# Performance work log

Measured on AMD Instinct MI355X. Metric: run time of the kernel, lower is better.

The kernel has to match this reference:

```python
import math
import jax, jax.numpy as jnp
import numpy as np

B, T, C, H = 1, 2048, 1024, 16
D = C // H
ROPE_THETA = 10000.0


def rope_sin_cos(t, d, theta, dtype=jnp.float32):
    # (T, D/2) sin/cos tables, standard RoPE frequencies
    inv_freq = 1.0 / (theta ** (jnp.arange(0, d, 2, dtype=jnp.float32) / d))
    ang = jnp.arange(t, dtype=jnp.float32)[:, None] * inv_freq[None, :]  # (T, D/2)
    return jnp.sin(ang).astype(dtype), jnp.cos(ang).astype(dtype)


def apply_rope(x, sin, cos):
    # x: (B, H, T, D); rotate interleaved even/odd pairs
    x1 = x[..., 0::2]
    x2 = x[..., 1::2]
    s = sin[None, None, :, :]
    c = cos[None, None, :, :]
    r1 = x1 * c - x2 * s
    r2 = x1 * s + x2 * c
    # interleave back to (..., D)
    return jnp.stack([r1, r2], axis=-1).reshape(x.shape)


def setup_inputs() -> dict:
    key = jax.random.key(0)
    k1, k2, k3 = jax.random.split(key, 3)
    x = jax.random.normal(k1, (B, T, C), dtype=jnp.float32)
    w_qkv = jax.random.normal(k2, (C, 3 * C), dtype=jnp.float32) * (1.0 / math.sqrt(C))
    w_proj = jax.random.normal(k3, (C, C), dtype=jnp.float32) * (1.0 / math.sqrt(C))
    return {"x": x, "w_qkv": w_qkv, "w_proj": w_proj}


def reference(x, w_qkv, w_proj):
    b, t, c = x.shape
    qkv = x @ w_qkv                               # (B, T, 3C)
    qkv = qkv.reshape(b, t, 3, H, D)
    q = qkv[:, :, 0].transpose(0, 2, 1, 3)        # (B, H, T, D)
    k = qkv[:, :, 1].transpose(0, 2, 1, 3)
    v = qkv[:, :, 2].transpose(0, 2, 1, 3)

    sin, cos = rope_sin_cos(t, D, ROPE_THETA, dtype=x.dtype)
    q = apply_rope(q, sin, cos)
    k = apply_rope(k, sin, cos)

    scores = jnp.einsum('bhqd,bhkd->bhqk', q, k) * (1.0 / math.sqrt(D))
    causal = jnp.tril(jnp.ones((t, t), dtype=bool))
    scores = jnp.where(causal[None, None, :, :], scores, jnp.finfo(scores.dtype).min)
    probs = jax.nn.softmax(scores, axis=-1)       # (B, H, T, T)
    out = jnp.einsum('bhqk,bhkd->bhqd', probs, v)
    out = out.transpose(0, 2, 1, 3).reshape(b, t, c)
    return out @ w_proj
```

## Files before the change

kernel.cpp:

```cpp
#include <hip/hip_runtime.h>
#include <math.h>

#define TT 2048
#define CC 1024
#define HH 16
#define DD 64
#define N3 3072

typedef unsigned short u16;
typedef __bf16 bf16x8 __attribute__((ext_vector_type(8)));
typedef float f32x4 __attribute__((ext_vector_type(4)));
typedef unsigned short u16x8 __attribute__((ext_vector_type(8)));
typedef const __attribute__((address_space(1))) void gv_t;
typedef __attribute__((address_space(3))) void lv_t;

__device__ __forceinline__ u16 bf16_rne(float f) {
  unsigned u = __float_as_uint(f);
  u += 0x7FFFu + ((u >> 16) & 1u);
  return (u16)(u >> 16);
}
__device__ __forceinline__ float bf16f(u16 h) {
  return __uint_as_float(((unsigned)h) << 16);
}
__device__ __forceinline__ bf16x8 ldfrag(const u16* p) {
  return __builtin_bit_cast(bf16x8, *(const u16x8*)p);
}
#if __has_builtin(__builtin_amdgcn_cvt_pk_bf16_f32)
__device__ __forceinline__ unsigned pk_bf16(float a, float b) {
  return __builtin_bit_cast(unsigned, __builtin_amdgcn_cvt_pk_bf16_f32(a, b));
}
#else
__device__ __forceinline__ unsigned pk_bf16(float a, float b) {
  return (unsigned)bf16_rne(a) | ((unsigned)bf16_rne(b) << 16);
}
#endif

__global__ __launch_bounds__(256) void k_prep(
    const float* __restrict__ x, const float* __restrict__ w_qkv,
    const float* __restrict__ w_proj, u16* __restrict__ xb,
    u16* __restrict__ wqkvT, u16* __restrict__ wprojT,
    float2* __restrict__ scos ) {
  __shared__ u16 tile[64][34];
  const int bi = blockIdx.x, tid = threadIdx.x;
  if (bi < 2048) {
    int i = bi * 256 + tid;
    float4 v = ((const float4*)x)[i];
    ushort4 r;
    r.x = bf16_rne(v.x); r.y = bf16_rne(v.y); r.z = bf16_rne(v.z); r.w = bf16_rne(v.w);
    ((ushort4*)xb)[i] = r;
    return;
  }
  if (bi >= 2048 + 1536 + 512) {
    int idx = (bi - 4096) * 256 + tid;
    int t = idx >> 5, i = idx & 31;
    float inv_freq = exp2f(-(float)(2 * i) * (1.0f / 64.0f) * 13.2877123795494f);
    float ang = (float)t * inv_freq;
    scos[idx] = make_float2(sinf(ang), cosf(ang));
    return;
  }
  const float* w; u16* wt; int K, N, n0, k0;
  if (bi < 2048 + 1536) {
    int b = bi - 2048; w = w_qkv; wt = wqkvT; K = CC; N = N3;
    k0 = (b / 96) * 64; n0 = (b % 96) * 32;
  } else {
    int b = bi - 3584; w = w_proj; wt = wprojT; K = CC; N = CC;
    k0 = (b >> 5) * 64; n0 = (b & 31) * 32;
  }
  const int tx = tid & 31, r0 = tid >> 5;
#pragma unroll
  for (int j = 0; j < 8; j++) {
    int k = r0 + j * 8;
    tile[k][tx] = bf16_rne(w[(size_t)(k0 + k) * N + n0 + tx]);
  }
  __syncthreads();
  const int kc = tid & 15, nr = tid >> 4;
#pragma unroll
  for (int jn = 0; jn < 2; jn++) {
    int n = nr + (jn << 4);
    ushort4 o;
    o.x = tile[kc * 4 + 0][n];
    o.y = tile[kc * 4 + 1][n];
    o.z = tile[kc * 4 + 2][n];
    o.w = tile[kc * 4 + 3][n];
    *(ushort4*)&wt[(size_t)(n0 + n) * K + k0 + kc * 4] = o;
  }
}

__device__ __forceinline__ bf16x8 rdsw(const u16* base, int rr, int c8) {
  return ldfrag(&base[rr * 64 + ((c8 ^ (rr & 7)) << 3)]);
}

__global__ __launch_bounds__(256) void k_gemm_qkv(
    const u16* __restrict__ A, const u16* __restrict__ Bt,
    const float2* __restrict__ scos , u16* __restrict__ qr,
    u16* __restrict__ kr, u16* __restrict__ vt, int M, int N, int K) {
  __shared__ u16 As[2][128 * 64];
  __shared__ u16 Bs[2][96 * 64];
  const int tid = threadIdx.x;
  const int lane = tid & 63, w = tid >> 6;
  const int col = lane & 15, quad = lane >> 4;
  const int wm = w >> 1, wn = w & 1;
  const int tm = blockIdx.y * 128, tn = blockIdx.x * 96;

  const int lr = lane >> 3;
  const int soff = ((lane & 7) ^ lr) << 3;

  f32x4 acc[12];
#pragma unroll
  for (int i = 0; i < 12; i++) acc[i] = (f32x4){0.f, 0.f, 0.f, 0.f};

  auto stage = [&](int k0, int buf) {
#pragma unroll
    for (int i = 0; i < 4; i++) {
      const int rbase = w * 32 + i * 8;
      __builtin_amdgcn_global_load_lds(
          (gv_t*)(A + (size_t)(tm + rbase + lr) * K + k0 + soff),
          (lv_t*)(&As[buf][rbase * 64]), 16, 0, 0);
    }
#pragma unroll
    for (int i = 0; i < 3; i++) {
      const int rbase = w * 24 + i * 8;
      __builtin_amdgcn_global_load_lds(
          (gv_t*)(Bt + (size_t)(tn + rbase + lr) * K + k0 + soff),
          (lv_t*)(&Bs[buf][rbase * 64]), 16, 0, 0);
    }
  };

  stage(0, 0);
  __syncthreads();
  const int NT = K / 64;
  for (int t = 0; t < NT; t++) {
    const int cur = t & 1;
    if (t + 1 < NT) stage((t + 1) * 64, cur ^ 1);
#pragma unroll
    for (int kk = 0; kk < 2; kk++) {
      bf16x8 af[4], bf[3];
#pragma unroll
      for (int mt = 0; mt < 4; mt++)
        af[mt] = rdsw(&As[cur][0], wm * 64 + mt * 16 + col, kk * 4 + quad);
#pragma unroll
      for (int nt = 0; nt < 3; nt++)
        bf[nt] = rdsw(&Bs[cur][0], wn * 48 + nt * 16 + col, kk * 4 + quad);
#pragma unroll
      for (int mt = 0; mt < 4; mt++)
#pragma unroll
        for (int nt = 0; nt < 3; nt++)
          acc[mt * 3 + nt] = __builtin_amdgcn_mfma_f32_16x16x32_bf16(af[mt], bf[nt], acc[mt * 3 + nt], 0, 0, 0);
    }
    __syncthreads();
  }
  u16* scr = ((u16*)As) + w * 1088;

  const int tb = tm + wm * 64;
#pragma unroll
  for (int nt = 0; nt < 3; nt++) {
    const int nn = tn + wn * 48 + nt * 16;
    const int slice = nn >> 10;
    const int hh = (nn >> 6) & 15;
    const int db = nn & 63;
    const int d = db + col;
    if (slice < 2) {
      u16* dst = (slice == 0) ? qr : kr;
      const bool ev = (col & 1) == 0;
      const int i = (db >> 1) + (col >> 1);
#pragma unroll
      for (int mt = 0; mt < 4; mt++)
#pragma unroll
        for (int r = 0; r < 4; r++) {
          int t = tb + mt * 16 + quad * 4 + r;
          float2 sc2 = scos[t * 32 + i];
          float e = acc[mt * 3 + nt][r];
          float pp = __shfl_xor(e, 1);
          float v = ev ? (e * sc2.y - pp * sc2.x) : (pp * sc2.x + e * sc2.y);
          dst[((size_t)(hh * TT + t) << 6) + d] = bf16_rne(v);
        }
    } else {
#pragma unroll
      for (int mt = 0; mt < 4; mt++)
#pragma unroll
        for (int r = 0; r < 4; r++)
          scr[col * 68 + mt * 16 + quad * 4 + r] = bf16_rne(acc[mt * 3 + nt][r]);
#pragma unroll
      for (int i = 0; i < 4; i++) {
        const int dl = quad + i * 4;
        const int tl = col * 4;
        ushort4 vv = *(const ushort4*)&scr[dl * 68 + tl];
        *(ushort4*)&vt[((size_t)(hh * DD + db + dl)) * TT + tb + tl] = vv;
      }
    }
  }
}

__global__ __launch_bounds__(256) void k_gemm_pj(
    const u16* __restrict__ A, const u16* __restrict__ Bt,
    float* __restrict__ C, int M, int N, int K) {
  __shared__ u16 As[2][64 * 64];
  __shared__ u16 Bs[2][64 * 64];
  const int tid = threadIdx.x;
  const int lane = tid & 63, w = tid >> 6;
  const int col = lane & 15, quad = lane >> 4;
  const int wm = w >> 1, wn = w & 1;
  const int tm = blockIdx.y * 64, tn = blockIdx.x * 64;

  const int lr = lane >> 3;
  const int soff = ((lane & 7) ^ lr) << 3;

  f32x4 acc[4];
#pragma unroll
  for (int i = 0; i < 4; i++) acc[i] = (f32x4){0.f, 0.f, 0.f, 0.f};

  auto stage = [&](int k0, int buf) {
#pragma unroll
    for (int i = 0; i < 2; i++) {
      const int rbase = w * 16 + i * 8;
      __builtin_amdgcn_global_load_lds(
          (gv_t*)(A + (size_t)(tm + rbase + lr) * K + k0 + soff),
          (lv_t*)(&As[buf][rbase * 64]), 16, 0, 0);
      __builtin_amdgcn_global_load_lds(
          (gv_t*)(Bt + (size_t)(tn + rbase + lr) * K + k0 + soff),
          (lv_t*)(&Bs[buf][rbase * 64]), 16, 0, 0);
    }
  };

  stage(0, 0);
  __syncthreads();
  const int NT = K / 64;
  for (int t = 0; t < NT; t++) {
    const int cur = t & 1;
    if (t + 1 < NT) stage((t + 1) * 64, cur ^ 1);
#pragma unroll
    for (int kk = 0; kk < 2; kk++) {
      bf16x8 af[2], bf[2];
#pragma unroll
      for (int mt = 0; mt < 2; mt++)
        af[mt] = rdsw(&As[cur][0], wm * 32 + mt * 16 + col, kk * 4 + quad);
#pragma unroll
      for (int nt = 0; nt < 2; nt++)
        bf[nt] = rdsw(&Bs[cur][0], wn * 32 + nt * 16 + col, kk * 4 + quad);
#pragma unroll
      for (int mt = 0; mt < 2; mt++)
#pragma unroll
        for (int nt = 0; nt < 2; nt++)
          acc[mt * 2 + nt] = __builtin_amdgcn_mfma_f32_16x16x32_bf16(af[mt], bf[nt], acc[mt * 2 + nt], 0, 0, 0);
    }
    __syncthreads();
  }
#pragma unroll
  for (int mt = 0; mt < 2; mt++)
#pragma unroll
    for (int nt = 0; nt < 2; nt++)
#pragma unroll
      for (int r = 0; r < 4; r++)
        C[(size_t)(tm + wm * 32 + mt * 16 + quad * 4 + r) * N + tn + wn * 32 + nt * 16 + col] =
            acc[mt * 2 + nt][r];
}

__global__ __launch_bounds__(256) void k_flash(
    const u16* __restrict__ qr, const u16* __restrict__ kr,
    const u16* __restrict__ vt, u16* __restrict__ attnb ) {
  __shared__ u16 Ks[2][64 * 64];
  __shared__ u16 Vs[2][64 * 64];
  __shared__ u16 Ps[4][16 * 64];

  const int tid = threadIdx.x;
  const int lane = tid & 63, wv = tid >> 6;
  const int col = lane & 15, quad = lane >> 4;

  const int bid = blockIdx.x;
  const int xcd = bid & 7, slot = bid >> 3;
  const int cu = slot & 31, half = slot >> 5;
  const int rank = half ? (63 - cu) : cu;
  const int sp = 31 - (rank >> 1);
  const int h = xcd * 2 + (rank & 1);
  const int q0 = sp * 64;
  const int nkt = sp + 1;

  const u16* Qh = qr + (size_t)h * TT * DD;
  const u16* Kh = kr + (size_t)h * TT * DD;
  const u16* Vh = vt + (size_t)h * DD * TT;

  const bf16x8 aq0 = ldfrag(&Qh[(size_t)(q0 + wv * 16 + col) * DD + quad * 8]);
  const bf16x8 aq1 = ldfrag(&Qh[(size_t)(q0 + wv * 16 + col) * DD + 32 + quad * 8]);

  const int lr = lane >> 3;
  const int srcoff = ((lane & 7) ^ lr) << 3;

  auto stage = [&](int j, int buf) {
    const int k0 = j * 64;
#pragma unroll
    for (int i = 0; i < 2; i++) {
      const int rbase = wv * 16 + i * 8;
      __builtin_amdgcn_global_load_lds(
          (gv_t*)(Kh + (size_t)(k0 + rbase + lr) * DD + srcoff),
          (lv_t*)(&Ks[buf][rbase * 64]), 16, 0, 0);
      __builtin_amdgcn_global_load_lds(
          (gv_t*)(Vh + (size_t)(rbase + lr) * TT + k0 + srcoff),
          (lv_t*)(&Vs[buf][rbase * 64]), 16, 0, 0);
    }
  };

  const f32x4 zero = {0.f, 0.f, 0.f, 0.f};
  f32x4 acc[4] = {zero, zero, zero, zero};
  float lpart[4] = {0.f, 0.f, 0.f, 0.f};
  u16* Pb = &Ps[wv][0];

  auto compute = [&](int k0j, const u16* Kt, const u16* Vt) {
    f32x4 sc[4];
#pragma unroll
    for (int nt = 0; nt < 4; nt++) {
      const int rr = nt * 16 + col;
      sc[nt] = __builtin_amdgcn_mfma_f32_16x16x32_bf16(aq0, rdsw(Kt, rr, quad), zero, 0, 0, 0);
      sc[nt] = __builtin_amdgcn_mfma_f32_16x16x32_bf16(aq1, rdsw(Kt, rr, 4 + quad), sc[nt], 0, 0, 0);
    }
    if (k0j == q0) {
#pragma unroll
      for (int nt = 0; nt < 4; nt++)
#pragma unroll
        for (int r = 0; r < 4; r++)
          if (nt * 16 + col > wv * 16 + quad * 4 + r) sc[nt][r] = -1e30f;
    }
#pragma unroll
    for (int nt = 0; nt < 4; nt++)
#pragma unroll
      for (int r = 0; r < 4; r++) {
        float p = exp2f(fmaf(sc[nt][r], 0.18033688f, -28.8539008f));
        sc[nt][r] = p;
        lpart[r] += p;
      }
#pragma unroll
    for (int nt = 0; nt < 4; nt++) {
      unsigned p01 = pk_bf16(sc[nt][0], sc[nt][1]);
      unsigned p23 = pk_bf16(sc[nt][2], sc[nt][3]);
      u16* base = Pb + quad * 4 * 64 + ((nt ^ quad) << 4) + col;
      base[0 * 64] = (u16)p01;
      base[1 * 64] = (u16)(p01 >> 16);
      base[2 * 64] = (u16)p23;
      base[3 * 64] = (u16)(p23 >> 16);
    }
#pragma unroll
    for (int kk = 0; kk < 2; kk++) {
      int sb = (kk * 2 + (quad >> 1)) ^ (col >> 2);
      bf16x8 ap = ldfrag(&Pb[col * 64 + (sb << 4) + ((quad & 1) << 3)]);
#pragma unroll
      for (int nt = 0; nt < 4; nt++)
        acc[nt] = __builtin_amdgcn_mfma_f32_16x16x32_bf16(
            ap, rdsw(Vt, nt * 16 + col, kk * 4 + quad), acc[nt], 0, 0, 0);
    }
  };

  stage(0, 0);
  for (int j = 0; j < nkt; j++) {
    const int buf = j & 1;
    __syncthreads();
    if (j + 1 < nkt) stage(j + 1, buf ^ 1);
    compute(j * 64, Ks[buf], Vs[buf]);
  }

#pragma unroll
  for (int o = 1; o < 16; o <<= 1)
#pragma unroll
    for (int r = 0; r < 4; r++) lpart[r] += __shfl_xor(lpart[r], o);
  float inv[4];
#pragma unroll
  for (int r = 0; r < 4; r++) inv[r] = 1.f / lpart[r];
#pragma unroll
  for (int nt = 0; nt < 4; nt++)
#pragma unroll
    for (int r = 0; r < 4; r++) {
      int q = q0 + wv * 16 + quad * 4 + r;
      attnb[(size_t)q * CC + h * DD + nt * 16 + col] = bf16_rne(acc[nt][r] * inv[r]);
    }
}

extern "C" void kernel_launch(void* const* d_in, const int* in_sizes, int n_in,
                              void* d_out, int out_size, void* d_ws, size_t ws_size,
                              hipStream_t stream) {
  const float* x      = (const float*)d_in[0];
  const float* w_qkv  = (const float*)d_in[1];
  const float* w_proj = (const float*)d_in[2];
  float* out = (float*)d_out;

  char* p = (char*)d_ws;
  u16* xb      = (u16*)p;    p += (size_t)TT * CC * 2;
  u16* wqkvT   = (u16*)p;    p += (size_t)N3 * CC * 2;
  u16* wprojT  = (u16*)p;    p += (size_t)CC * CC * 2;
  float2* scos = (float2*)p; p += (size_t)TT * 32 * 8;
  u16* qr      = (u16*)p;    p += (size_t)HH * TT * DD * 2;
  u16* kr      = (u16*)p;    p += (size_t)HH * TT * DD * 2;
  u16* vt      = (u16*)p;    p += (size_t)HH * DD * TT * 2;
  u16* attnb   = (u16*)p;    p += (size_t)TT * CC * 2;

  k_prep<<<2048 + 1536 + 512 + 256, 256, 0, stream>>>(x, w_qkv, w_proj, xb, wqkvT, wprojT, scos);
  k_gemm_qkv<<<dim3(N3 / 96, TT / 128), 256, 0, stream>>>(xb, wqkvT, scos, qr, kr, vt, TT, N3, CC);
  k_flash<<<512, 256, 0, stream>>>(qr, kr, vt, attnb);
  k_gemm_pj<<<dim3(CC / 64, TT / 64), 256, 0, stream>>>(attnb, wprojT, out, TT, CC, CC);
}
```

Measured before the change: 145.0 us.

## Split flash attention into 32-row query blocks with two-way KV split per block

Each flash-attention block now handles 32 query rows instead of 64, and the grid doubles to 1024 blocks. Inside a block, two wave pairs take alternating 64-key tiles and combine partial accumulators and row sums through LDS at the end. The aim is finer-grained causal load balancing and more parallelism per head. In exchange it drops the double-buffered prefetch overlap, since loads and compute for each pair of tiles now sit between two barriers, and it adds a reduction step through LDS plus redundant K/V loads across the extra blocks.

New measurement: 136.0 us. -6.2%, faster.

```diff
diff --git a/kernel.cpp b/kernel.cpp
--- a/kernel.cpp
+++ b/kernel.cpp
@@ -268,43 +268,33 @@
 
   const int bid = blockIdx.x;
   const int xcd = bid & 7, slot = bid >> 3;
-  const int cu = slot & 31, half = slot >> 5;
-  const int rank = half ? (63 - cu) : cu;
-  const int sp = 31 - (rank >> 1);
+  const int cu = slot & 31, tier = slot >> 5;
+  const int rank = (tier & 1) ? (tier * 32 + (31 - cu)) : (tier * 32 + cu);
   const int h = xcd * 2 + (rank & 1);
-  const int q0 = sp * 64;
-  const int nkt = sp + 1;
+  const int s = rank >> 1;
+  const int q0 = s * 32;
+  const int nkt = (s >> 1) + 1;
+  const int tdiag = s >> 1;
+
+  const int qh = wv & 1;
+  const int kp = wv >> 1;
 
   const u16* Qh = qr + (size_t)h * TT * DD;
   const u16* Kh = kr + (size_t)h * TT * DD;
   const u16* Vh = vt + (size_t)h * DD * TT;
 
-  const bf16x8 aq0 = ldfrag(&Qh[(size_t)(q0 + wv * 16 + col) * DD + quad * 8]);
-  const bf16x8 aq1 = ldfrag(&Qh[(size_t)(q0 + wv * 16 + col) * DD + 32 + quad * 8]);
+  const bf16x8 aq0 = ldfrag(&Qh[(size_t)(q0 + qh * 16 + col) * DD + quad * 8]);
+  const bf16x8 aq1 = ldfrag(&Qh[(size_t)(q0 + qh * 16 + col) * DD + 32 + quad * 8]);
 
   const int lr = lane >> 3;
   const int srcoff = ((lane & 7) ^ lr) << 3;
-
-  auto stage = [&](int j, int buf) {
-    const int k0 = j * 64;
-#pragma unroll
-    for (int i = 0; i < 2; i++) {
-      const int rbase = wv * 16 + i * 8;
-      __builtin_amdgcn_global_load_lds(
-          (gv_t*)(Kh + (size_t)(k0 + rbase + lr) * DD + srcoff),
-          (lv_t*)(&Ks[buf][rbase * 64]), 16, 0, 0);
-      __builtin_amdgcn_global_load_lds(
-          (gv_t*)(Vh + (size_t)(rbase + lr) * TT + k0 + srcoff),
-          (lv_t*)(&Vs[buf][rbase * 64]), 16, 0, 0);
-    }
-  };
 
   const f32x4 zero = {0.f, 0.f, 0.f, 0.f};
   f32x4 acc[4] = {zero, zero, zero, zero};
   float lpart[4] = {0.f, 0.f, 0.f, 0.f};
   u16* Pb = &Ps[wv][0];
 
-  auto compute = [&](int k0j, const u16* Kt, const u16* Vt) {
+  auto compute = [&](int t, const u16* Kt, const u16* Vt) {
     f32x4 sc[4];
 #pragma unroll
     for (int nt = 0; nt < 4; nt++) {
@@ -312,12 +302,12 @@
       sc[nt] = __builtin_amdgcn_mfma_f32_16x16x32_bf16(aq0, rdsw(Kt, rr, quad), zero, 0, 0, 0);
       sc[nt] = __builtin_amdgcn_mfma_f32_16x16x32_bf16(aq1, rdsw(Kt, rr, 4 + quad), sc[nt], 0, 0, 0);
     }
-    if (k0j == q0) {
+    if (t == tdiag) {
 #pragma unroll
       for (int nt = 0; nt < 4; nt++)
 #pragma unroll
         for (int r = 0; r < 4; r++)
-          if (nt * 16 + col > wv * 16 + quad * 4 + r) sc[nt][r] = -1e30f;
+          if (t * 64 + nt * 16 + col > q0 + qh * 16 + quad * 4 + r) sc[nt][r] = -1e30f;
     }
 #pragma unroll
     for (int nt = 0; nt < 4; nt++)
@@ -348,28 +338,65 @@
     }
   };
 
-  stage(0, 0);
-  for (int j = 0; j < nkt; j++) {
-    const int buf = j & 1;
+  const int nw = (nkt + 1) >> 1;
+  for (int w = 0; w < nw; w++) {
     __syncthreads();
-    if (j + 1 < nkt) stage(j + 1, buf ^ 1);
-    compute(j * 64, Ks[buf], Vs[buf]);
-  }
-
-#pragma unroll
-  for (int o = 1; o < 16; o <<= 1)
-#pragma unroll
-    for (int r = 0; r < 4; r++) lpart[r] += __shfl_xor(lpart[r], o);
-  float inv[4];
-#pragma unroll
-  for (int r = 0; r < 4; r++) inv[r] = 1.f / lpart[r];
-#pragma unroll
-  for (int nt = 0; nt < 4; nt++)
-#pragma unroll
-    for (int r = 0; r < 4; r++) {
-      int q = q0 + wv * 16 + quad * 4 + r;
-      attnb[(size_t)q * CC + h * DD + nt * 16 + col] = bf16_rne(acc[nt][r] * inv[r]);
-    }
+#pragma unroll
+    for (int j = 0; j < 2; j++) {
+      const int t = 2 * w + j;
+      if (t < nkt) {
+#pragma unroll
+        for (int i = 0; i < 2; i++) {
+          const int rbase = wv * 16 + i * 8;
+          __builtin_amdgcn_global_load_lds(
+              (gv_t*)(Kh + (size_t)(t * 64 + rbase + lr) * DD + srcoff),
+              (lv_t*)(&Ks[j][rbase * 64]), 16, 0, 0);
+          __builtin_amdgcn_global_load_lds(
+              (gv_t*)(Vh + (size_t)(rbase + lr) * TT + t * 64 + srcoff),
+              (lv_t*)(&Vs[j][rbase * 64]), 16, 0, 0);
+        }
+      }
+    }
+    __syncthreads();
+    const int t = 2 * w + kp;
+    if (t < nkt) compute(t, Ks[kp], Vs[kp]);
+  }
+
+  float* mbuf = (float*)&Ks[0][0];
+  __syncthreads();
+  if (kp == 1) {
+    float* mb = mbuf + qh * 1344;
+#pragma unroll
+    for (int i = 0; i < 4; i++)
+#pragma unroll
+      for (int r = 0; r < 4; r++) mb[lane * 20 + i * 4 + r] = acc[i][r];
+#pragma unroll
+    for (int r = 0; r < 4; r++) mb[lane * 20 + 16 + r] = lpart[r];
+  }
+  __syncthreads();
+  if (kp == 0) {
+    float* mb = mbuf + qh * 1344;
+#pragma unroll
+    for (int i = 0; i < 4; i++)
+#pragma unroll
+      for (int r = 0; r < 4; r++) acc[i][r] += mb[lane * 20 + i * 4 + r];
+#pragma unroll
+    for (int r = 0; r < 4; r++) lpart[r] += mb[lane * 20 + 16 + r];
+#pragma unroll
+    for (int o = 1; o < 16; o <<= 1)
+#pragma unroll
+      for (int r = 0; r < 4; r++) lpart[r] += __shfl_xor(lpart[r], o);
+    float inv[4];
+#pragma unroll
+    for (int r = 0; r < 4; r++) inv[r] = 1.f / lpart[r];
+#pragma unroll
+    for (int nt = 0; nt < 4; nt++)
+#pragma unroll
+      for (int r = 0; r < 4; r++) {
+        int q = q0 + qh * 16 + quad * 4 + r;
+        attnb[(size_t)q * CC + h * DD + nt * 16 + col] = bf16_rne(acc[nt][r] * inv[r]);
+      }
+  }
 }
 
 extern "C" void kernel_launch(void* const* d_in, const int* in_sizes, int n_in,
@@ -392,6 +419,6 @@
 
   k_prep<<<2048 + 1536 + 512 + 256, 256, 0, stream>>>(x, w_qkv, w_proj, xb, wqkvT, wprojT, scos);
   k_gemm_qkv<<<dim3(N3 / 96, TT / 128), 256, 0, stream>>>(xb, wqkvT, scos, qr, kr, vt, TT, N3, CC);
-  k_flash<<<512, 256, 0, stream>>>(qr, kr, vt, attnb);
+  k_flash<<<1024, 256, 0, stream>>>(qr, kr, vt, attnb);
   k_gemm_pj<<<dim3(CC / 64, TT / 64), 256, 0, stream>>>(attnb, wprojT, out, TT, CC, CC);
 }
```
